# Kernel tuning notes

Measured on AMD Instinct MI355X. Metric: run time of the kernel, lower is better.

## Reference

```python
import jax, jax.numpy as jnp
import numpy as np

T = 4096   # reference sequence length (concatenated virtual samples)
L = 4096   # modality sequence length
D_Q = 64   # reference feature dim
D_QK = 128 # projected query/key dim (before add_one -> 129)
D_V = 128  # value dim
N_IDS = 8  # number of virtual samples encoded in idx


def setup_inputs() -> dict:
    key = jax.random.key(0)
    ks = jax.random.split(key, 20)
    inp = {}
    inp['ref_data'] = jax.random.normal(ks[0], (1, 1, T, D_Q), jnp.float32)
    inp['ref_time'] = jnp.sort(jax.random.uniform(ks[1], (1, T), jnp.float32), axis=-1)
    inp['ref_idx'] = jnp.sort(jax.random.randint(ks[2], (T,), 0, N_IDS))
    inp['m1_data'] = jax.random.normal(ks[3], (1, 1, L, 130), jnp.float32)
    inp['m1_time'] = jnp.sort(jax.random.uniform(ks[4], (1, L), jnp.float32), axis=-1)
    inp['m1_idx'] = jnp.sort(jax.random.randint(ks[5], (L,), 0, N_IDS))
    inp['m2_data'] = jax.random.normal(ks[6], (1, 1, L, 66), jnp.float32)
    inp['m2_time'] = jnp.sort(jax.random.uniform(ks[7], (1, L), jnp.float32), axis=-1)
    inp['m2_idx'] = jnp.sort(jax.random.randint(ks[8], (L,), 0, N_IDS))
    s = 0.05
    inp['Wq'] = jax.random.normal(ks[9], (D_Q, D_QK), jnp.float32) * s
    inp['bq'] = jnp.zeros((D_QK,), jnp.float32)
    inp['Wk1'] = jax.random.normal(ks[10], (1, D_QK), jnp.float32) * s
    inp['bk1'] = jnp.zeros((D_QK,), jnp.float32)
    inp['Wv1'] = jax.random.normal(ks[11], (128, D_V), jnp.float32) * s
    inp['bv1'] = jnp.zeros((D_V,), jnp.float32)
    inp['Wk2'] = jax.random.normal(ks[12], (1, D_QK), jnp.float32) * s
    inp['bk2'] = jnp.zeros((D_QK,), jnp.float32)
    inp['Wv2'] = jax.random.normal(ks[13], (64, D_V), jnp.float32) * s
    inp['bv2'] = jnp.zeros((D_V,), jnp.float32)
    inp['log_tau1'] = jnp.zeros((), jnp.float32)  # log(init_tau=1)
    inp['log_tau2'] = jnp.zeros((), jnp.float32)
    return inp


def _add_one_q(x):  # add_one(x, dim=1): append ones on last axis
    return jnp.concatenate([x, jnp.ones(x.shape[:-1] + (1,), x.dtype)], axis=-1)


def _feat_k(x):  # add_one(x, dim=0): [ones, -x]
    return jnp.concatenate([jnp.ones(x.shape[:-1] + (1,), x.dtype), -x], axis=-1)


def _uni_attn(Q, mdata, q_t, kv_t, q_idx, kv_idx, Wk, bk, Wv, bv, log_tau):
    # qk_type='time': keys from last feature (timestamp), values from data[..., :-2]
    K = _feat_k(mdata[..., -1:] @ Wk + bk)          # (1,1,L,d_qk+1)
    V = mdata[..., :-2] @ Wv + bv                   # (1,1,L,d_v)
    tau = jnp.exp(log_tau)
    # gaussian weight: -(Q.K)^2 / tau
    A = -jnp.square(jnp.einsum('nhtc,nhlc->nhtl', Q, K)) / tau  # (1,1,T,L)
    causal = (q_t[:, :, None] >= kv_t[:, None, :]).astype(Q.dtype)[:, None]  # (1,1,T,L)
    neg_inf = jnp.array(-jnp.inf, Q.dtype)
    bm = jnp.where(q_idx[None, :, None] == kv_idx[None, None, :], jnp.zeros((), Q.dtype), neg_inf)  # (1,T,L)
    fully_masked = jnp.all(jnp.isneginf(bm), axis=-1, keepdims=True)
    safe = jnp.where(fully_masked, jnp.zeros((), Q.dtype), bm)[:, None]  # (1,1,T,L)
    A = jax.nn.softmax(A * causal + safe, axis=-1) * causal
    return jnp.einsum('nhtl,nhlc->nhtc', A, V)      # (1,1,T,d_v)


def reference(ref_data, ref_time, m1_data, m1_time, m2_data, m2_time,
              Wq, bq, Wk1, bk1, Wv1, bv1, Wk2, bk2, Wv2, bv2,
              log_tau1, log_tau2, ref_idx, m1_idx, m2_idx):
    Q = _add_one_q(ref_data @ Wq + bq)  # (1,1,T,d_qk+1)
    y1 = _uni_attn(Q, m1_data, ref_time, m1_time, ref_idx, m1_idx, Wk1, bk1, Wv1, bv1, log_tau1)
    y2 = _uni_attn(Q, m2_data, ref_time, m2_time, ref_idx, m2_idx, Wk2, bk2, Wv2, bv2, log_tau2)
    return jnp.concatenate([y1, y2], axis=-1)  # (1,1,T,2*d_v)
```

## Files before the change

### kernel.cpp

```cpp
#include <hip/hip_runtime.h>
#include <hip/hip_bf16.h>

#define TQ 4096
#define LK 4096
#define QT 16
#define NSPLIT 8
#define NSUB (NSPLIT * 2)
#define CHJ 16
#define PB 32
#define PQ (TQ / PB)

template<bool BF> __device__ __forceinline__ float ld(const void* p, int i);
template<> __device__ __forceinline__ float ld<true>(const void* p, int i) {
    return __bfloat162float(((const __hip_bfloat16*)p)[i]);
}
template<> __device__ __forceinline__ float ld<false>(const void* p, int i) {
    return ((const float*)p)[i];
}
template<bool BF> __device__ __forceinline__ float2 ld2(const void* p, int i);
template<> __device__ __forceinline__ float2 ld2<false>(const void* p, int i) {
    return *(const float2*)((const float*)p + i);
}
template<> __device__ __forceinline__ float2 ld2<true>(const void* p, int i) {
    float2 r; r.x = ld<true>(p, i); r.y = ld<true>(p, i + 1); return r;
}
template<bool BF> __device__ __forceinline__ float4 ld4(const void* p, int i);
template<> __device__ __forceinline__ float4 ld4<false>(const void* p, int i) {
    return *(const float4*)((const float*)p + i);
}
template<> __device__ __forceinline__ float4 ld4<true>(const void* p, int i) {
    float4 r; r.x = ld<true>(p, i); r.y = ld<true>(p, i + 1);
    r.z = ld<true>(p, i + 2); r.w = ld<true>(p, i + 3); return r;
}
template<bool BF> __device__ __forceinline__ void st4(void* p, int i, float4 v);
template<> __device__ __forceinline__ void st4<true>(void* p, int i, float4 v) {
    __hip_bfloat16* o = (__hip_bfloat16*)p + i;
    o[0] = __float2bfloat16(v.x); o[1] = __float2bfloat16(v.y);
    o[2] = __float2bfloat16(v.z); o[3] = __float2bfloat16(v.w);
}
template<> __device__ __forceinline__ void st4<false>(void* p, int i, float4 v) {
    *(float4*)((float*)p + i) = v;
}

__device__ __forceinline__ bool sniff_bf16(const void* ref_time) {
    const int lane = threadIdx.x & 63;
    bool ok = true;
    if (lane < 32) {
        float v = __bfloat162float(((const __hip_bfloat16*)ref_time)[2 * lane]);
        ok = (v >= 0.0f) && (v <= 1.0f);
    }
    return __ballot(ok) == ~0ULL;
}

__device__ int lb_int(const int* arr, int n, int key) {
    int lo = 0, hi = n;
    while (lo < hi) { int mid = (lo + hi) >> 1; if (arr[mid] < key) lo = mid + 1; else hi = mid; }
    return lo;
}
__device__ int ub_int(const int* arr, int n, int key) {
    int lo = 0, hi = n;
    while (lo < hi) { int mid = (lo + hi) >> 1; if (arr[mid] <= key) lo = mid + 1; else hi = mid; }
    return lo;
}

template<bool BF>
__device__ void prep_body(
    const void* ref_data, const void* ref_time, const int* ref_idx,
    const void* m1_time, const int* m1_idx, const void* m2_time, const int* m2_idx,
    const void* Wq, const void* bq,
    const void* Wk1, const void* bk1, const void* Wk2, const void* bk2,
    float* alpha1, float* beta1, float* alpha2, float* beta2,
    int* c1, int* s1, int* e1, int* c2, int* s2, int* e2)
{
    __shared__ float ut[64][4];
    __shared__ float cst[4];
    __shared__ int tabs[4][8];

    const int tid = threadIdx.x;
    const int i = tid >> 2, r = tid & 3;

    {
        const void* w = (r == 0) ? Wk1 : (r == 1) ? bk1 : (r == 2) ? Wk2 : bk2;
        const bool isA = (r & 1);
        float acc = isA ? ld<BF>(Wq, i * 128) : 0.0f;
        const float sgn = isA ? -1.0f : 1.0f;
        #pragma unroll 4
        for (int d = 1; d < 128; ++d)
            acc = fmaf(sgn * ld<BF>(Wq, i * 128 + d), ld<BF>(w, d - 1), acc);
        ut[i][r] = acc;
    }
    if (tid < 4) {
        const void* w = (tid == 0) ? Wk1 : (tid == 1) ? bk1 : (tid == 2) ? Wk2 : bk2;
        const bool isA = (tid & 1);
        float c = isA ? ld<BF>(bq, 0) : 0.0f;
        const float sgn = isA ? -1.0f : 1.0f;
        #pragma unroll 4
        for (int d = 1; d < 128; ++d)
            c = fmaf(sgn * ld<BF>(bq, d), ld<BF>(w, d - 1), c);
        c += sgn * ld<BF>(w, 127);
        cst[tid] = c;
    }
    if (tid >= 4 && tid < 36) {
        const int k = tid - 4;
        const int sid = k & 7, rest = k >> 3;
        const int modk = rest & 1, kind = rest >> 1;
        const int* arr = modk ? m2_idx : m1_idx;
        tabs[modk * 2 + kind][sid] = kind ? ub_int(arr, LK, sid) : lb_int(arr, LK, sid);
    }
    __syncthreads();

    const int q = tid & 127;
    const int t = blockIdx.x * PQ + q;
    if (tid < 128) {
        float4 acc = {cst[0], cst[1], cst[2], cst[3]};
        #pragma unroll
        for (int ii = 0; ii < 64; ii += 4) {
            const float4 rv = ld4<BF>(ref_data, t * 64 + ii);
            const float4 u0 = *(const float4*)ut[ii + 0];
            const float4 u1 = *(const float4*)ut[ii + 1];
            const float4 u2 = *(const float4*)ut[ii + 2];
            const float4 u3 = *(const float4*)ut[ii + 3];
            acc.x = fmaf(rv.x, u0.x, fmaf(rv.y, u1.x, fmaf(rv.z, u2.x, fmaf(rv.w, u3.x, acc.x))));
            acc.y = fmaf(rv.x, u0.y, fmaf(rv.y, u1.y, fmaf(rv.z, u2.y, fmaf(rv.w, u3.y, acc.y))));
            acc.z = fmaf(rv.x, u0.z, fmaf(rv.y, u1.z, fmaf(rv.z, u2.z, fmaf(rv.w, u3.z, acc.z))));
            acc.w = fmaf(rv.x, u0.w, fmaf(rv.y, u1.w, fmaf(rv.z, u2.w, fmaf(rv.w, u3.w, acc.w))));
        }
        beta1[t] = acc.x; alpha1[t] = acc.y;
        beta2[t] = acc.z; alpha2[t] = acc.w;
    } else {
        const float qt = ld<BF>(ref_time, t);
        const int g = ref_idx[t];
        int lo1 = 0, hi1 = LK, lo2 = 0, hi2 = LK;
        #pragma unroll
        for (int it = 0; it < 13; ++it) {
            const int mA = min((lo1 + hi1) >> 1, LK - 1);
            const int mB = min((lo2 + hi2) >> 1, LK - 1);
            const float v1 = ld<BF>(m1_time, mA);
            const float v2 = ld<BF>(m2_time, mB);
            if (lo1 < hi1) { if (v1 <= qt) lo1 = mA + 1; else hi1 = mA; }
            if (lo2 < hi2) { if (v2 <= qt) lo2 = mB + 1; else hi2 = mB; }
        }
        c1[t] = lo1; c2[t] = lo2;
        s1[t] = tabs[0][g]; e1[t] = tabs[1][g];
        s2[t] = tabs[2][g]; e2[t] = tabs[3][g];
    }
}

__global__ __launch_bounds__(256) void prep_kernel(
    const void* ref_data, const void* ref_time, const int* ref_idx,
    const void* m1_time, const int* m1_idx, const void* m2_time, const int* m2_idx,
    const void* Wq, const void* bq,
    const void* Wk1, const void* bk1, const void* Wk2, const void* bk2,
    float* alpha1, float* beta1, float* alpha2, float* beta2,
    int* c1, int* s1, int* e1, int* c2, int* s2, int* e2)
{
    if (sniff_bf16(ref_time))
        prep_body<true>(ref_data, ref_time, ref_idx, m1_time, m1_idx, m2_time, m2_idx,
                        Wq, bq, Wk1, bk1, Wk2, bk2,
                        alpha1, beta1, alpha2, beta2, c1, s1, e1, c2, s2, e2);
    else
        prep_body<false>(ref_data, ref_time, ref_idx, m1_time, m1_idx, m2_time, m2_idx,
                         Wq, bq, Wk1, bk1, Wk2, bk2,
                         alpha1, beta1, alpha2, beta2, c1, s1, e1, c2, s2, e2);
}

template<bool BF, int K, int DM>
__device__ void vproj_wave(const void* md, const void* Wv, const void* bv,
                           float* V, float* X, int rows0)
{
    const int lane = threadIdx.x & 63;
    const int cT = lane & 31;
    const int rG = lane >> 5;
    const int r0 = rows0 + rG * 2;
    const int c4 = cT * 4;

    const float4 bb = ld4<BF>(bv, c4);
    float4 acc[2] = {bb, bb};

    #pragma unroll 4
    for (int k = 0; k < K; k += 4) {
        const float4 w0 = ld4<BF>(Wv, (k + 0) * 128 + c4);
        const float4 w1 = ld4<BF>(Wv, (k + 1) * 128 + c4);
        const float4 w2 = ld4<BF>(Wv, (k + 2) * 128 + c4);
        const float4 w3 = ld4<BF>(Wv, (k + 3) * 128 + c4);
        float2 alo[2], ahi[2];
        #pragma unroll
        for (int r = 0; r < 2; ++r) {
            alo[r] = ld2<BF>(md, (r0 + r) * DM + k);
            ahi[r] = ld2<BF>(md, (r0 + r) * DM + k + 2);
        }
        #pragma unroll
        for (int r = 0; r < 2; ++r) {
            acc[r].x = fmaf(alo[r].x, w0.x, fmaf(alo[r].y, w1.x, fmaf(ahi[r].x, w2.x, fmaf(ahi[r].y, w3.x, acc[r].x))));
            acc[r].y = fmaf(alo[r].x, w0.y, fmaf(alo[r].y, w1.y, fmaf(ahi[r].x, w2.y, fmaf(ahi[r].y, w3.y, acc[r].y))));
            acc[r].z = fmaf(alo[r].x, w0.z, fmaf(alo[r].y, w1.z, fmaf(ahi[r].x, w2.z, fmaf(ahi[r].y, w3.z, acc[r].z))));
            acc[r].w = fmaf(alo[r].x, w0.w, fmaf(alo[r].y, w1.w, fmaf(ahi[r].x, w2.w, fmaf(ahi[r].y, w3.w, acc[r].w))));
        }
    }
    #pragma unroll
    for (int r = 0; r < 2; ++r)
        *(float4*)&V[(size_t)(r0 + r) * 128 + c4] = acc[r];
    if (rG == 0 && cT < 4)
        X[rows0 + cT] = ld<BF>(md, (rows0 + cT) * DM + DM - 1);
}

__global__ __launch_bounds__(64) void vproj_kernel(
    const void* __restrict__ ref_time,
    const void* m1_data, const void* Wv1, const void* bv1,
    const void* m2_data, const void* Wv2, const void* bv2,
    float* V1, float* V2, float* X1, float* X2)
{
    const int rows0 = blockIdx.x * 4;
    const int mod = blockIdx.y;
    const bool bf = sniff_bf16(ref_time);
    if (mod == 0) {
        if (bf) vproj_wave<true, 128, 130>(m1_data, Wv1, bv1, V1, X1, rows0);
        else    vproj_wave<false, 128, 130>(m1_data, Wv1, bv1, V1, X1, rows0);
    } else {
        if (bf) vproj_wave<true, 64, 66>(m2_data, Wv2, bv2, V2, X2, rows0);
        else    vproj_wave<false, 64, 66>(m2_data, Wv2, bv2, V2, X2, rows0);
    }
}

__global__ __launch_bounds__(128) void attn_kernel(
    const void* __restrict__ ref_time,
    const float* __restrict__ alpha1, const float* __restrict__ beta1,
    const float* __restrict__ alpha2, const float* __restrict__ beta2,
    const int* __restrict__ c1, const int* __restrict__ s1, const int* __restrict__ e1,
    const int* __restrict__ c2, const int* __restrict__ s2, const int* __restrict__ e2,
    const float* __restrict__ V1, const float* __restrict__ V2,
    const float* __restrict__ X1, const float* __restrict__ X2,
    const void* log_tau1, const void* log_tau2,
    float* __restrict__ Opart, float* __restrict__ Zpart)
{
    __shared__ float sW[2][CHJ * QT];

    const int tid = threadIdx.x;
    const int wid = tid >> 6, lane = tid & 63;
    const int t0 = blockIdx.x * QT, zb = blockIdx.y, mod = blockIdx.z;

    const bool bf = sniff_bf16(ref_time);
    const float* alpha = mod ? alpha2 : alpha1;
    const float* beta  = mod ? beta2  : beta1;
    const int* cA = mod ? c2 : c1;
    const int* sA = mod ? s2 : s1;
    const int* eA = mod ? e2 : e1;
    const float* V = mod ? V2 : V1;
    const float* X = mod ? X2 : X1;
    const void* ltp = mod ? log_tau2 : log_tau1;
    const float scale = __expf(-(bf ? ld<true>(ltp, 0) : ld<false>(ltp, 0)));

    const int q = lane & 15;
    const int t = t0 + q;
    int s = sA[t], e = eA[t];
    const int c = cA[t];
    if (s == e) { s = 0; e = LK; }
    const int cm = min(c, e);
    const float al = alpha[t], be = beta[t];

    int es = (cm > s) ? s : 0x7fffffff;
    int ec = (cm > s) ? cm : 0;
    #pragma unroll
    for (int o = 1; o < 64; o <<= 1) {
        es = min(es, __shfl_xor(es, o));
        ec = max(ec, __shfl_xor(ec, o));
    }
    int jlo = es, jhi = ec;
    if (jlo > jhi) { jlo = 0; jhi = 0; }
    const int W = jhi - jlo;
    const int chunk = (W + NSUB - 1) / NSUB;
    const int sub = zb * 2 + wid;
    const int lo = jlo + sub * chunk;
    int hi = min(jhi, lo + chunk); if (hi < lo) hi = lo;

    const int cT = lane & 31, qG = lane >> 5;
    const int jj = lane >> 4;
    float4 acc[8] = {{0,0,0,0},{0,0,0,0},{0,0,0,0},{0,0,0,0},
                     {0,0,0,0},{0,0,0,0},{0,0,0,0},{0,0,0,0}};
    float zacc = 0.0f;
    float* myW = sW[wid];
    const float4* __restrict__ Vg = (const float4*)V;

    for (int base = lo; base < hi; base += CHJ) {
        const int jm = min(CHJ, hi - base);
        __asm__ volatile("s_waitcnt lgkmcnt(0)" ::: "memory");
        #pragma unroll
        for (int p = 0; p < 4; ++p) {
            const int jr = jj * 4 + p;
            const int j = base + jr;
            const bool ok = (jr < jm) && (j >= s) && (j < cm);
            const float x = X[min(j, LK - 1)];
            const float qk = fmaf(-be, x, al);
            const float w = ok ? __expf(-(qk * qk) * scale) : 0.0f;
            myW[jr * QT + q] = w;
            zacc += w;
        }
        __asm__ volatile("s_waitcnt lgkmcnt(0)" ::: "memory");
        #pragma unroll 4
        for (int j = 0; j < jm; ++j) {
            const float4 v = Vg[(base + j) * 32 + cT];
            const float4* wv = (const float4*)&myW[j * QT + qG * 8];
            const float4 wA = wv[0], wB = wv[1];
            acc[0].x = fmaf(wA.x, v.x, acc[0].x); acc[0].y = fmaf(wA.x, v.y, acc[0].y);
            acc[0].z = fmaf(wA.x, v.z, acc[0].z); acc[0].w = fmaf(wA.x, v.w, acc[0].w);
            acc[1].x = fmaf(wA.y, v.x, acc[1].x); acc[1].y = fmaf(wA.y, v.y, acc[1].y);
            acc[1].z = fmaf(wA.y, v.z, acc[1].z); acc[1].w = fmaf(wA.y, v.w, acc[1].w);
            acc[2].x = fmaf(wA.z, v.x, acc[2].x); acc[2].y = fmaf(wA.z, v.y, acc[2].y);
            acc[2].z = fmaf(wA.z, v.z, acc[2].z); acc[2].w = fmaf(wA.z, v.w, acc[2].w);
            acc[3].x = fmaf(wA.w, v.x, acc[3].x); acc[3].y = fmaf(wA.w, v.y, acc[3].y);
            acc[3].z = fmaf(wA.w, v.z, acc[3].z); acc[3].w = fmaf(wA.w, v.w, acc[3].w);
            acc[4].x = fmaf(wB.x, v.x, acc[4].x); acc[4].y = fmaf(wB.x, v.y, acc[4].y);
            acc[4].z = fmaf(wB.x, v.z, acc[4].z); acc[4].w = fmaf(wB.x, v.w, acc[4].w);
            acc[5].x = fmaf(wB.y, v.x, acc[5].x); acc[5].y = fmaf(wB.y, v.y, acc[5].y);
            acc[5].z = fmaf(wB.y, v.z, acc[5].z); acc[5].w = fmaf(wB.y, v.w, acc[5].w);
            acc[6].x = fmaf(wB.z, v.x, acc[6].x); acc[6].y = fmaf(wB.z, v.y, acc[6].y);
            acc[6].z = fmaf(wB.z, v.z, acc[6].z); acc[6].w = fmaf(wB.z, v.w, acc[6].w);
            acc[7].x = fmaf(wB.w, v.x, acc[7].x); acc[7].y = fmaf(wB.w, v.y, acc[7].y);
            acc[7].z = fmaf(wB.w, v.z, acc[7].z); acc[7].w = fmaf(wB.w, v.w, acc[7].w);
        }
    }

    float z = zacc;
    z += __shfl_xor(z, 16);
    z += __shfl_xor(z, 32);

    const int part = sub * 2 + mod;
    float4* Og = (float4*)Opart;
    #pragma unroll
    for (int r = 0; r < 8; ++r)
        Og[((size_t)(part << 12) + (t0 + qG * 8 + r)) * 32 + cT] = acc[r];
    if (lane < 16) Zpart[(part << 12) + t0 + lane] = z;
}

__global__ __launch_bounds__(256) void finish_kernel(
    const void* __restrict__ ref_time,
    const int* __restrict__ c1, const int* __restrict__ s1, const int* __restrict__ e1,
    const int* __restrict__ c2, const int* __restrict__ s2, const int* __restrict__ e2,
    const float* __restrict__ Zpart, const float* __restrict__ Opart,
    void* __restrict__ out)
{
    const bool bf = sniff_bf16(ref_time);
    const int idx = blockIdx.x * 256 + threadIdx.x;
    const int t = idx >> 6;
    const int rem = idx & 63;
    const int mod = rem >> 5;
    const int c4 = rem & 31;

    const int* cA = mod ? c2 : c1;
    const int* sA = mod ? s2 : s1;
    const int* eA = mod ? e2 : e1;
    int s = sA[t], e = eA[t];
    const int c = cA[t];
    if (s == e) { s = 0; e = LK; }
    const int nnc = (e > c) ? (e - max(s, c)) : 0;

    float Z = (float)nnc;
    float4 o = {0, 0, 0, 0};
    const float4* Og = (const float4*)Opart;
    #pragma unroll
    for (int zi = 0; zi < NSUB; ++zi) {
        const int part = zi * 2 + mod;
        Z += Zpart[(part << 12) + t];
        const float4 p = Og[((size_t)(part << 12) + t) * 32 + c4];
        o.x += p.x; o.y += p.y; o.z += p.z; o.w += p.w;
    }
    const float inv = 1.0f / fmaxf(Z, 1.0e-20f);
    o.x *= inv; o.y *= inv; o.z *= inv; o.w *= inv;
    if (bf) st4<true>(out, t * 256 + mod * 128 + c4 * 4, o);
    else    st4<false>(out, t * 256 + mod * 128 + c4 * 4, o);
}

extern "C" void kernel_launch(void* const* d_in, const int* in_sizes, int n_in,
                              void* d_out, int out_size, void* d_ws, size_t ws_size,
                              hipStream_t stream)
{
    const void* ref_data = d_in[0];
    const void* ref_time = d_in[1];
    const int*  ref_idx  = (const int*)d_in[2];
    const void* m1_data  = d_in[3];
    const void* m1_time  = d_in[4];
    const int*  m1_idx   = (const int*)d_in[5];
    const void* m2_data  = d_in[6];
    const void* m2_time  = d_in[7];
    const int*  m2_idx   = (const int*)d_in[8];
    const void* Wq  = d_in[9];
    const void* bq  = d_in[10];
    const void* Wk1 = d_in[11];
    const void* bk1 = d_in[12];
    const void* Wv1 = d_in[13];
    const void* bv1 = d_in[14];
    const void* Wk2 = d_in[15];
    const void* bk2 = d_in[16];
    const void* Wv2 = d_in[17];
    const void* bv2 = d_in[18];
    const void* log_tau1 = d_in[19];
    const void* log_tau2 = d_in[20];

    float* ws = (float*)d_ws;
    float* alpha1 = ws + 0 * TQ;
    float* beta1  = ws + 1 * TQ;
    float* alpha2 = ws + 2 * TQ;
    float* beta2  = ws + 3 * TQ;
    int*   c1 = (int*)(ws + 4 * TQ);
    int*   c2 = (int*)(ws + 5 * TQ);
    int*   s1 = (int*)(ws + 6 * TQ);
    int*   e1 = (int*)(ws + 7 * TQ);
    int*   s2 = (int*)(ws + 8 * TQ);
    int*   e2 = (int*)(ws + 9 * TQ);
    float* X1 = ws + 10 * TQ;
    float* X2 = ws + 11 * TQ;
    float* V1 = ws + 12 * TQ;
    float* V2 = V1 + (size_t)LK * 128;
    float* Zpart = V2 + (size_t)LK * 128;
    float* Opart = Zpart + 32 * TQ;

    prep_kernel<<<dim3(PB), dim3(256), 0, stream>>>(
        ref_data, ref_time, ref_idx, m1_time, m1_idx, m2_time, m2_idx,
        Wq, bq, Wk1, bk1, Wk2, bk2,
        alpha1, beta1, alpha2, beta2, c1, s1, e1, c2, s2, e2);

    vproj_kernel<<<dim3(LK / 4, 2), dim3(64), 0, stream>>>(
        ref_time, m1_data, Wv1, bv1, m2_data, Wv2, bv2, V1, V2, X1, X2);

    attn_kernel<<<dim3(TQ / QT, NSPLIT, 2), dim3(128), 0, stream>>>(
        ref_time, alpha1, beta1, alpha2, beta2, c1, s1, e1, c2, s2, e2,
        V1, V2, X1, X2, log_tau1, log_tau2, Opart, Zpart);

    finish_kernel<<<dim3(TQ * 2 * 32 / 256), dim3(256), 0, stream>>>(
        ref_time, c1, s1, e1, c2, s2, e2, Zpart, Opart, (void*)d_out);
}
```

Measured before the change: 182.3 us.

## Merge prep and value projection kernels; halve attention splits with in-block reduction

```diff
diff --git a/kernel.cpp b/kernel.cpp
--- a/kernel.cpp
+++ b/kernel.cpp
@@ -4,11 +4,11 @@
 #define TQ 4096
 #define LK 4096
 #define QT 16
-#define NSPLIT 8
-#define NSUB (NSPLIT * 2)
+#define NSPLIT 4
 #define CHJ 16
 #define PB 32
 #define PQ (TQ / PB)
+#define VPB 512
 
 template<bool BF> __device__ __forceinline__ float ld(const void* p, int i);
 template<> __device__ __forceinline__ float ld<true>(const void* p, int i) {
@@ -64,7 +64,7 @@
 }
 
 template<bool BF>
-__device__ void prep_body(
+__device__ void prep_part(
     const void* ref_data, const void* ref_time, const int* ref_idx,
     const void* m1_time, const int* m1_idx, const void* m2_time, const int* m2_idx,
     const void* Wq, const void* bq,
@@ -146,24 +146,6 @@
     }
 }
 
-__global__ __launch_bounds__(256) void prep_kernel(
-    const void* ref_data, const void* ref_time, const int* ref_idx,
-    const void* m1_time, const int* m1_idx, const void* m2_time, const int* m2_idx,
-    const void* Wq, const void* bq,
-    const void* Wk1, const void* bk1, const void* Wk2, const void* bk2,
-    float* alpha1, float* beta1, float* alpha2, float* beta2,
-    int* c1, int* s1, int* e1, int* c2, int* s2, int* e2)
-{
-    if (sniff_bf16(ref_time))
-        prep_body<true>(ref_data, ref_time, ref_idx, m1_time, m1_idx, m2_time, m2_idx,
-                        Wq, bq, Wk1, bk1, Wk2, bk2,
-                        alpha1, beta1, alpha2, beta2, c1, s1, e1, c2, s2, e2);
-    else
-        prep_body<false>(ref_data, ref_time, ref_idx, m1_time, m1_idx, m2_time, m2_idx,
-                         Wq, bq, Wk1, bk1, Wk2, bk2,
-                         alpha1, beta1, alpha2, beta2, c1, s1, e1, c2, s2, e2);
-}
-
 template<bool BF, int K, int DM>
 __device__ void vproj_wave(const void* md, const void* Wv, const void* bv,
                            float* V, float* X, int rows0)
@@ -204,22 +186,53 @@
         X[rows0 + cT] = ld<BF>(md, (rows0 + cT) * DM + DM - 1);
 }
 
-__global__ __launch_bounds__(64) void vproj_kernel(
-    const void* __restrict__ ref_time,
-    const void* m1_data, const void* Wv1, const void* bv1,
-    const void* m2_data, const void* Wv2, const void* bv2,
+template<bool BF>
+__device__ void pv_body(
+    const void* ref_data, const void* ref_time, const int* ref_idx,
+    const void* m1_data, const void* m1_time, const int* m1_idx,
+    const void* m2_data, const void* m2_time, const int* m2_idx,
+    const void* Wq, const void* bq,
+    const void* Wk1, const void* bk1, const void* Wk2, const void* bk2,
+    const void* Wv1, const void* bv1, const void* Wv2, const void* bv2,
+    float* alpha1, float* beta1, float* alpha2, float* beta2,
+    int* c1, int* s1, int* e1, int* c2, int* s2, int* e2,
     float* V1, float* V2, float* X1, float* X2)
 {
-    const int rows0 = blockIdx.x * 4;
-    const int mod = blockIdx.y;
-    const bool bf = sniff_bf16(ref_time);
-    if (mod == 0) {
-        if (bf) vproj_wave<true, 128, 130>(m1_data, Wv1, bv1, V1, X1, rows0);
-        else    vproj_wave<false, 128, 130>(m1_data, Wv1, bv1, V1, X1, rows0);
+    if (blockIdx.x < PB) {
+        prep_part<BF>(ref_data, ref_time, ref_idx, m1_time, m1_idx, m2_time, m2_idx,
+                      Wq, bq, Wk1, bk1, Wk2, bk2,
+                      alpha1, beta1, alpha2, beta2, c1, s1, e1, c2, s2, e2);
     } else {
-        if (bf) vproj_wave<true, 64, 66>(m2_data, Wv2, bv2, V2, X2, rows0);
-        else    vproj_wave<false, 64, 66>(m2_data, Wv2, bv2, V2, X2, rows0);
-    }
+        const int vb = blockIdx.x - PB;
+        const int mod = vb >> 8;
+        const int wid = threadIdx.x >> 6;
+        const int rows0 = (vb & 255) * 16 + wid * 4;
+        if (mod == 0) vproj_wave<BF, 128, 130>(m1_data, Wv1, bv1, V1, X1, rows0);
+        else          vproj_wave<BF, 64, 66>(m2_data, Wv2, bv2, V2, X2, rows0);
+    }
+}
+
+__global__ __launch_bounds__(256) void pv_kernel(
+    const void* ref_data, const void* ref_time, const int* ref_idx,
+    const void* m1_data, const void* m1_time, const int* m1_idx,
+    const void* m2_data, const void* m2_time, const int* m2_idx,
+    const void* Wq, const void* bq,
+    const void* Wk1, const void* bk1, const void* Wk2, const void* bk2,
+    const void* Wv1, const void* bv1, const void* Wv2, const void* bv2,
+    float* alpha1, float* beta1, float* alpha2, float* beta2,
+    int* c1, int* s1, int* e1, int* c2, int* s2, int* e2,
+    float* V1, float* V2, float* X1, float* X2)
+{
+    if (sniff_bf16(ref_time))
+        pv_body<true>(ref_data, ref_time, ref_idx, m1_data, m1_time, m1_idx,
+                      m2_data, m2_time, m2_idx, Wq, bq, Wk1, bk1, Wk2, bk2,
+                      Wv1, bv1, Wv2, bv2, alpha1, beta1, alpha2, beta2,
+                      c1, s1, e1, c2, s2, e2, V1, V2, X1, X2);
+    else
+        pv_body<false>(ref_data, ref_time, ref_idx, m1_data, m1_time, m1_idx,
+                       m2_data, m2_time, m2_idx, Wq, bq, Wk1, bk1, Wk2, bk2,
+                       Wv1, bv1, Wv2, bv2, alpha1, beta1, alpha2, beta2,
+                       c1, s1, e1, c2, s2, e2, V1, V2, X1, X2);
 }
 
 __global__ __launch_bounds__(128) void attn_kernel(
@@ -234,6 +247,8 @@
     float* __restrict__ Opart, float* __restrict__ Zpart)
 {
     __shared__ float sW[2][CHJ * QT];
+    __shared__ float sO[QT * 128];
+    __shared__ float sZm[QT];
 
     const int tid = threadIdx.x;
     const int wid = tid >> 6, lane = tid & 63;
@@ -268,7 +283,7 @@
     int jlo = es, jhi = ec;
     if (jlo > jhi) { jlo = 0; jhi = 0; }
     const int W = jhi - jlo;
-    const int chunk = (W + NSUB - 1) / NSUB;
+    const int chunk = (W + NSPLIT * 2 - 1) / (NSPLIT * 2);
     const int sub = zb * 2 + wid;
     const int lo = jlo + sub * chunk;
     int hi = min(jhi, lo + chunk); if (hi < lo) hi = lo;
@@ -324,12 +339,25 @@
     z += __shfl_xor(z, 16);
     z += __shfl_xor(z, 32);
 
-    const int part = sub * 2 + mod;
-    float4* Og = (float4*)Opart;
-    #pragma unroll
-    for (int r = 0; r < 8; ++r)
-        Og[((size_t)(part << 12) + (t0 + qG * 8 + r)) * 32 + cT] = acc[r];
-    if (lane < 16) Zpart[(part << 12) + t0 + lane] = z;
+    const int part = zb * 2 + mod;
+    if (wid == 0) {
+        #pragma unroll
+        for (int r = 0; r < 8; ++r)
+            *(float4*)&sO[(qG * 8 + r) * 128 + cT * 4] = acc[r];
+        if (lane < 16) sZm[lane] = z;
+    }
+    __syncthreads();
+    if (wid == 1) {
+        float4* Og = (float4*)Opart;
+        #pragma unroll
+        for (int r = 0; r < 8; ++r) {
+            const float4 o0 = *(const float4*)&sO[(qG * 8 + r) * 128 + cT * 4];
+            float4 o = acc[r];
+            o.x += o0.x; o.y += o0.y; o.z += o0.z; o.w += o0.w;
+            Og[((size_t)(part << 12) + (t0 + qG * 8 + r)) * 32 + cT] = o;
+        }
+        if (lane < 16) Zpart[(part << 12) + t0 + lane] = z + sZm[lane];
+    }
 }
 
 __global__ __launch_bounds__(256) void finish_kernel(
@@ -358,8 +386,8 @@
     float4 o = {0, 0, 0, 0};
     const float4* Og = (const float4*)Opart;
     #pragma unroll
-    for (int zi = 0; zi < NSUB; ++zi) {
-        const int part = zi * 2 + mod;
+    for (int zb = 0; zb < NSPLIT; ++zb) {
+        const int part = zb * 2 + mod;
         Z += Zpart[(part << 12) + t];
         const float4 p = Og[((size_t)(part << 12) + t) * 32 + c4];
         o.x += p.x; o.y += p.y; o.z += p.z; o.w += p.w;
@@ -412,15 +440,13 @@
     float* V1 = ws + 12 * TQ;
     float* V2 = V1 + (size_t)LK * 128;
     float* Zpart = V2 + (size_t)LK * 128;
-    float* Opart = Zpart + 32 * TQ;
-
-    prep_kernel<<<dim3(PB), dim3(256), 0, stream>>>(
-        ref_data, ref_time, ref_idx, m1_time, m1_idx, m2_time, m2_idx,
-        Wq, bq, Wk1, bk1, Wk2, bk2,
-        alpha1, beta1, alpha2, beta2, c1, s1, e1, c2, s2, e2);
-
-    vproj_kernel<<<dim3(LK / 4, 2), dim3(64), 0, stream>>>(
-        ref_time, m1_data, Wv1, bv1, m2_data, Wv2, bv2, V1, V2, X1, X2);
+    float* Opart = Zpart + 8 * TQ;
+
+    pv_kernel<<<dim3(PB + VPB), dim3(256), 0, stream>>>(
+        ref_data, ref_time, ref_idx, m1_data, m1_time, m1_idx,
+        m2_data, m2_time, m2_idx, Wq, bq, Wk1, bk1, Wk2, bk2,
+        Wv1, bv1, Wv2, bv2, alpha1, beta1, alpha2, beta2,
+        c1, s1, e1, c2, s2, e2, V1, V2, X1, X2);
 
     attn_kernel<<<dim3(TQ / QT, NSPLIT, 2), dim3(128), 0, stream>>>(
         ref_time, alpha1, beta1, alpha2, beta2, c1, s1, e1, c2, s2, e2,
```

Measured after the change: 164.1 us. 10.0% less time.
